# Kernel optimization log

Measured on AMD Instinct MI355X. Metric: run time of the kernel, lower is better.

The kernel has to match this reference:

```python
import jax, jax.numpy as jnp
import numpy as np

PH, PW = 7, 7      # pool_shape
SCALE = 1.0        # spatial_scale of PrRoIPool2D


def _tent_int(t):
    """Antiderivative of the bilinear tent kernel max(0, 1-|t|), clipped.
    Integral of tent from -inf to t."""
    t = jnp.clip(t, -1.0, 1.0)
    return jnp.where(t < 0.0, 0.5 * (t + 1.0) ** 2, 1.0 - 0.5 * (1.0 - t) ** 2)


def _axis_weights(lo, hi, n_bins, size):
    """Exact per-pixel integration weights along one axis.
    lo, hi: [R] roi edges. Returns (w [R, n_bins, size], bin_size [R]).
    w[r,k,i] = integral over bin k of tent(x - i) dx, so that
    sum_i F[i] * w[r,k,i] is the exact integral of the linearly
    interpolated signal F over bin k (Precise RoI Pooling)."""
    binsz = (hi - lo) / n_bins                       # [R]
    k = jnp.arange(n_bins, dtype=lo.dtype)
    a = lo[:, None] + k[None, :] * binsz[:, None]    # [R, n_bins] bin starts
    b = a + binsz[:, None]                           # bin ends
    i = jnp.arange(size, dtype=lo.dtype)             # pixel coordinates
    w = _tent_int(b[:, :, None] - i[None, None, :]) - _tent_int(a[:, :, None] - i[None, None, :])
    return w, binsz


def setup_inputs() -> dict:
    key = jax.random.key(0)
    k1, k2, k3, k4, k5 = jax.random.split(key, 5)
    B, C, H, W = 8, 64, 64, 64
    N = 512  # rois per leading dim; total R = N * B = 4096
    feature = jax.random.normal(k1, (B, C, H, W), dtype=jnp.float32)
    bidx = jax.random.randint(k2, (N, B, 1, 1), 0, B).astype(jnp.float32)
    x1 = jax.random.uniform(k3, (N, B, 1, 1), minval=0.0, maxval=W - 12.0)
    y1 = jax.random.uniform(k4, (N, B, 1, 1), minval=0.0, maxval=H - 12.0)
    wh = jax.random.uniform(k5, (N, B, 1, 1, 2), minval=4.0, maxval=12.0)
    x2 = x1 + wh[..., 0]
    y2 = y1 + wh[..., 1]
    rois = jnp.stack([bidx, x1, y1, x2, y2], axis=-1)  # [N, B, 1, 1, 5]
    return {"feature": feature, "rois": rois}


def reference(feature, rois):
    B, C, H, W = feature.shape
    # rois.permute([1,0,2,3,4]).reshape(-1, 5)
    r = jnp.transpose(rois, (1, 0, 2, 3, 4)).reshape(-1, 5)  # [R, 5]
    bidx = r[:, 0].astype(jnp.int32)
    x1 = r[:, 1] * SCALE
    y1 = r[:, 2] * SCALE
    x2 = r[:, 3] * SCALE
    y2 = r[:, 4] * SCALE

    wx, bw = _axis_weights(x1, x2, PW, W)  # [R, PW, W], [R]
    wy, bh = _axis_weights(y1, y2, PH, H)  # [R, PH, H], [R]

    # Route each ROI to its feature-batch entry without materializing
    # a [R, C, H, W] gather: fold the batch one-hot into the y-weights.
    onehot = (bidx[:, None] == jnp.arange(B)[None, :]).astype(feature.dtype)  # [R, B]
    wy_b = wy[:, :, None, :] * onehot[:, None, :, None]                      # [R, PH, B, H]

    tmp = jnp.einsum('rubi,bcij->rucj', wy_b, feature)  # [R, PH, C, W]
    integ = jnp.einsum('rucj,rvj->rcuv', tmp, wx)       # [R, C, PH, PW]

    area = jnp.maximum(bw * bh, 0.0)[:, None, None, None]
    bins = jnp.where(area > 0, integ / jnp.maximum(area, 1e-12), 0.0)

    # AvgPool2d(pool_shape) over the full (PH, PW) grid -> [R, C, 1, 1]
    out = jnp.mean(bins, axis=(2, 3), keepdims=True)
    return out
```

## Files before the change

kernel.cpp:

```cpp
#include <hip/hip_runtime.h>

constexpr int B = 8, C = 64, H = 64, W = 64;
constexpr int N = 512;
constexpr int R = N * B;
constexpr int HW = H * W;

__device__ __forceinline__ float tent_int(float t) {
    t = fminf(1.0f, fmaxf(-1.0f, t));
    float u = t + 1.0f;
    float v = 1.0f - t;
    return (t < 0.0f) ? 0.5f * u * u : 1.0f - 0.5f * v * v;
}

__device__ __forceinline__ float bf_lo(unsigned int u) {
    union { unsigned int i; float f; } c; c.i = u << 16; return c.f;
}
__device__ __forceinline__ float bf_hi(unsigned int u) {
    union { unsigned int i; float f; } c; c.i = u & 0xFFFF0000u; return c.f;
}
__device__ __forceinline__ unsigned short f2bf(float x) {
    union { float f; unsigned int i; } c; c.f = x;
    unsigned int r = c.i + 0x7FFFu + ((c.i >> 16) & 1u);
    return (unsigned short)(r >> 16);
}

__global__ __launch_bounds__(256) void transpose_kernel(
    const float* __restrict__ in,
    unsigned short* __restrict__ out)
{
    __shared__ float tile[64][65];
    const int b  = blockIdx.x >> 6;
    const int tp = (blockIdx.x & 63) * 64;
    const int t  = threadIdx.x;
    const int tq = t >> 6;
    const int tl = t & 63;

    const float* src = in + (size_t)b * C * HW;
    #pragma unroll
    for (int s = 0; s < 16; ++s) {
        int c = s * 4 + tq;
        tile[c][tl] = src[(size_t)c * HW + tp + tl];
    }
    __syncthreads();
    unsigned short* dst = out + ((size_t)b * HW + tp) * C;
    #pragma unroll
    for (int s = 0; s < 16; ++s) {
        int p = s * 4 + tq;
        dst[(size_t)p * C + tl] = f2bf(tile[tl][p]);
    }
}

__global__ __launch_bounds__(64) void prroi_main(
    const unsigned short* __restrict__ ft,
    const float* __restrict__ rois,
    float* __restrict__ out)
{
    const int r    = blockIdx.x;
    const int lane = threadIdx.x & 63;
    const int pg   = lane >> 3;
    const int cg   = lane & 7;

    const int bo = r >> 9;
    const int n  = r & 511;
    const float* rp = rois + ((size_t)n * B + bo) * 5;

    const int   b  = (int)rp[0];
    const float x1 = rp[1], y1 = rp[2], x2 = rp[3], y2 = rp[4];

    const int i_lo = max(0, (int)ceilf(y1 - 1.0f));
    const int i_hi = min(H - 1, (int)floorf(y2 + 1.0f));
    const int j_lo = max(0, (int)ceilf(x1 - 1.0f));
    const int j_hi = min(W - 1, (int)floorf(x2 + 1.0f));
    const int ny = i_hi - i_lo + 1;
    const int nx = j_hi - j_lo + 1;
    const int nk = (nx + 7) >> 3;

    float wx[2];
    int   coff[2];
    #pragma unroll
    for (int k = 0; k < 2; ++k) {
        const int  jj    = k * 8 + pg;
        const int  j     = j_lo + jj;
        const bool valid = (jj < nx);
        const float jf   = (float)j;
        wx[k]   = valid ? (tent_int(x2 - jf) - tent_int(x1 - jf)) : 0.0f;
        coff[k] = min(j, W - 1) * C + cg * 8;
    }

    float acc[8] = {0.f, 0.f, 0.f, 0.f, 0.f, 0.f, 0.f, 0.f};
    const unsigned short* fb = ft + ((size_t)b * HW + (size_t)i_lo * W) * C;
    for (int ii = 0; ii < ny; ++ii) {
        const float fi = (float)(i_lo + ii);
        const float wy = tent_int(y2 - fi) - tent_int(y1 - fi);
        const unsigned short* rowp = fb + (size_t)ii * (W * C);
        #pragma unroll 2
        for (int k = 0; k < nk; ++k) {
            const uint4 u = *reinterpret_cast<const uint4*>(rowp + coff[k]);
            const float w = wy * wx[k];
            acc[0] = fmaf(w, bf_lo(u.x), acc[0]);
            acc[1] = fmaf(w, bf_hi(u.x), acc[1]);
            acc[2] = fmaf(w, bf_lo(u.y), acc[2]);
            acc[3] = fmaf(w, bf_hi(u.y), acc[3]);
            acc[4] = fmaf(w, bf_lo(u.z), acc[4]);
            acc[5] = fmaf(w, bf_hi(u.z), acc[5]);
            acc[6] = fmaf(w, bf_lo(u.w), acc[6]);
            acc[7] = fmaf(w, bf_hi(u.w), acc[7]);
        }
    }

    #pragma unroll
    for (int e = 0; e < 8; ++e) {
        acc[e] += __shfl_xor(acc[e], 8);
        acc[e] += __shfl_xor(acc[e], 16);
        acc[e] += __shfl_xor(acc[e], 32);
    }

    const float prod  = (x2 - x1) * (y2 - y1);
    const float scale = (prod > 0.0f) ? (1.0f / fmaxf(prod, 49e-12f)) : 0.0f;

    if (lane < 8) {
        float* op = out + (size_t)r * C + lane * 8;
        float4 lo = make_float4(acc[0] * scale, acc[1] * scale,
                                acc[2] * scale, acc[3] * scale);
        float4 hi = make_float4(acc[4] * scale, acc[5] * scale,
                                acc[6] * scale, acc[7] * scale);
        *reinterpret_cast<float4*>(op)     = lo;
        *reinterpret_cast<float4*>(op + 4) = hi;
    }
}

__global__ __launch_bounds__(64) void prroi_fallback(
    const float* __restrict__ feature, const float* __restrict__ rois,
    float* __restrict__ out)
{
    const int r  = blockIdx.x;
    const int bo = r / N;
    const int n  = r - bo * N;
    const float* rp = rois + ((size_t)n * B + bo) * 5;
    const float x1 = rp[1], y1 = rp[2], x2 = rp[3], y2 = rp[4];
    const int b = (int)rp[0];
    int i_lo = max(0, (int)ceilf(y1 - 1.0f));
    int i_hi = min(H - 1, (int)floorf(y2 + 1.0f));
    int j_lo = max(0, (int)ceilf(x1 - 1.0f));
    int j_hi = min(W - 1, (int)floorf(x2 + 1.0f));
    const int ny = i_hi - i_lo + 1;
    const int nx = j_hi - j_lo + 1;
    __shared__ float sWy[16], sWx[16];
    const int t = threadIdx.x;
    if (t < 16) {
        int i = i_lo + t;
        sWy[t] = (t < ny) ? (tent_int(y2 - (float)i) - tent_int(y1 - (float)i)) : 0.0f;
    } else if (t < 32) {
        int tt = t - 16, j = j_lo + tt;
        sWx[tt] = (tt < nx) ? (tent_int(x2 - (float)j) - tent_int(x1 - (float)j)) : 0.0f;
    }
    __syncthreads();
    const float* fb = feature + ((size_t)b * C + t) * HW;
    float acc = 0.0f;
    for (int ii = 0; ii < ny; ++ii) {
        const float* row = fb + (size_t)(i_lo + ii) * W + j_lo;
        float rowsum = 0.0f;
        for (int jj = 0; jj < nx; ++jj) rowsum = fmaf(sWx[jj], row[jj], rowsum);
        acc = fmaf(sWy[ii], rowsum, acc);
    }
    const float bw = (x2 - x1) * (1.0f / 7.0f), bh = (y2 - y1) * (1.0f / 7.0f);
    const float area = fmaxf(bw * bh, 0.0f);
    out[(size_t)r * C + t] = (area > 0.0f) ? (acc / (49.0f * fmaxf(area, 1e-12f))) : 0.0f;
}

extern "C" void kernel_launch(void* const* d_in, const int* in_sizes, int n_in,
                              void* d_out, int out_size, void* d_ws, size_t ws_size,
                              hipStream_t stream) {
    const float* feature = (const float*)d_in[0];
    const float* rois    = (const float*)d_in[1];
    float* out           = (float*)d_out;

    const size_t need = (size_t)B * HW * C * sizeof(unsigned short);
    if (ws_size >= need) {
        unsigned short* ft = (unsigned short*)d_ws;
        transpose_kernel<<<B * (HW / 64), 256, 0, stream>>>(feature, ft);
        prroi_main<<<R, 64, 0, stream>>>(ft, rois, out);
    } else {
        prroi_fallback<<<R, 64, 0, stream>>>(feature, rois, out);
    }
}
```

Baseline: 71.35 us.

## Fuse transpose and pooling into one cooperative kernel with grid sync

Merges the bf16 channel-last transpose and the PrRoI pooling into a single cooperative kernel of 1024 blocks of 256 threads. Each block transposes a 32-pixel tile, then does a grid-wide sync before each of its four wavefronts pools one ROI. This removes a second kernel launch and the gap between the two kernels. In exchange it adds a grid barrier and a threadfence, needs every block to be resident at once, and falls back to the two-kernel path if the cooperative launch fails.

```diff
diff --git a/kernel.cpp b/kernel.cpp
--- a/kernel.cpp
+++ b/kernel.cpp
@@ -1,4 +1,7 @@
 #include <hip/hip_runtime.h>
+#include <hip/hip_cooperative_groups.h>
+
+namespace cg = cooperative_groups;
 
 constexpr int B = 8, C = 64, H = 64, W = 64;
 constexpr int N = 512;
@@ -22,6 +25,112 @@
     union { float f; unsigned int i; } c; c.f = x;
     unsigned int r = c.i + 0x7FFFu + ((c.i >> 16) & 1u);
     return (unsigned short)(r >> 16);
+}
+
+__global__ __launch_bounds__(256, 4) void prroi_fused(
+    const float* __restrict__ feature,
+    const float* __restrict__ rois,
+    unsigned short* __restrict__ ft,
+    float* __restrict__ out)
+{
+    __shared__ float tile[64][33];
+    {
+        const int b  = blockIdx.x >> 7;
+        const int tp = (blockIdx.x & 127) * 32;
+        const int t  = threadIdx.x;
+        const int tq8  = t >> 5;
+        const int tl32 = t & 31;
+        const float* src = feature + (size_t)b * C * HW;
+        #pragma unroll
+        for (int s = 0; s < 8; ++s) {
+            int c = s * 8 + tq8;
+            tile[c][tl32] = src[(size_t)c * HW + tp + tl32];
+        }
+        __syncthreads();
+        unsigned short* dst = ft + ((size_t)b * HW + tp) * C;
+        const int tq4  = t >> 6;
+        const int tl64 = t & 63;
+        #pragma unroll
+        for (int s = 0; s < 8; ++s) {
+            int p = s * 4 + tq4;
+            dst[(size_t)p * C + tl64] = f2bf(tile[tl64][p]);
+        }
+    }
+    __threadfence();
+    cg::this_grid().sync();
+
+    const int r    = blockIdx.x * 4 + (threadIdx.x >> 6);
+    const int lane = threadIdx.x & 63;
+    const int pg   = lane >> 3;
+    const int cg_  = lane & 7;
+
+    const int bo = r >> 9;
+    const int n  = r & 511;
+    const float* rp = rois + ((size_t)n * B + bo) * 5;
+
+    const int   b  = (int)rp[0];
+    const float x1 = rp[1], y1 = rp[2], x2 = rp[3], y2 = rp[4];
+
+    const int i_lo = max(0, (int)ceilf(y1 - 1.0f));
+    const int i_hi = min(H - 1, (int)floorf(y2 + 1.0f));
+    const int j_lo = max(0, (int)ceilf(x1 - 1.0f));
+    const int j_hi = min(W - 1, (int)floorf(x2 + 1.0f));
+    const int ny = i_hi - i_lo + 1;
+    const int nx = j_hi - j_lo + 1;
+    const int nk = (nx + 7) >> 3;
+
+    float wx[2];
+    int   coff[2];
+    #pragma unroll
+    for (int k = 0; k < 2; ++k) {
+        const int  jj    = k * 8 + pg;
+        const int  j     = j_lo + jj;
+        const bool valid = (jj < nx);
+        const float jf   = (float)j;
+        wx[k]   = valid ? (tent_int(x2 - jf) - tent_int(x1 - jf)) : 0.0f;
+        coff[k] = min(j, W - 1) * C + cg_ * 8;
+    }
+
+    float acc[8] = {0.f, 0.f, 0.f, 0.f, 0.f, 0.f, 0.f, 0.f};
+    const unsigned short* fb = ft + ((size_t)b * HW + (size_t)i_lo * W) * C;
+    for (int ii = 0; ii < ny; ++ii) {
+        const float fi = (float)(i_lo + ii);
+        const float wy = tent_int(y2 - fi) - tent_int(y1 - fi);
+        const unsigned short* rowp = fb + (size_t)ii * (W * C);
+        #pragma unroll 2
+        for (int k = 0; k < nk; ++k) {
+            const uint4 u = *reinterpret_cast<const uint4*>(rowp + coff[k]);
+            const float w = wy * wx[k];
+            acc[0] = fmaf(w, bf_lo(u.x), acc[0]);
+            acc[1] = fmaf(w, bf_hi(u.x), acc[1]);
+            acc[2] = fmaf(w, bf_lo(u.y), acc[2]);
+            acc[3] = fmaf(w, bf_hi(u.y), acc[3]);
+            acc[4] = fmaf(w, bf_lo(u.z), acc[4]);
+            acc[5] = fmaf(w, bf_hi(u.z), acc[5]);
+            acc[6] = fmaf(w, bf_lo(u.w), acc[6]);
+            acc[7] = fmaf(w, bf_hi(u.w), acc[7]);
+        }
+    }
+
+    #pragma unroll
+    for (int e = 0; e < 8; ++e) {
+        acc[e] += __shfl_xor(acc[e], 8);
+        acc[e] += __shfl_xor(acc[e], 16);
+        acc[e] += __shfl_xor(acc[e], 32);
+    }
+
+    const float prod  = (x2 - x1) * (y2 - y1);
+    const float scale = (prod > 0.0f) ? (1.0f / fmaxf(prod, 49e-12f)) : 0.0f;
+
+    if (lane < 8) {
+        float* op = out + (size_t)r * C + lane * 8;
+        float4 lo = make_float4(acc[0] * scale, acc[1] * scale,
+                                acc[2] * scale, acc[3] * scale);
+        float4 hi = make_float4(acc[4] * scale, acc[5] * scale,
+                                acc[6] * scale, acc[7] * scale);
+        *reinterpret_cast<float4*>(op)     = lo;
+        *reinterpret_cast<float4*>(op + 4) = hi;
+    }
 }
 
 __global__ __launch_bounds__(256) void transpose_kernel(
@@ -58,7 +167,7 @@
     const int r    = blockIdx.x;
     const int lane = threadIdx.x & 63;
     const int pg   = lane >> 3;
-    const int cg   = lane & 7;
+    const int cg_  = lane & 7;
 
     const int bo = r >> 9;
     const int n  = r & 511;
@@ -84,7 +193,7 @@
         const bool valid = (jj < nx);
         const float jf   = (float)j;
         wx[k]   = valid ? (tent_int(x2 - jf) - tent_int(x1 - jf)) : 0.0f;
-        coff[k] = min(j, W - 1) * C + cg * 8;
+        coff[k] = min(j, W - 1) * C + cg_ * 8;
     }
 
     float acc[8] = {0.f, 0.f, 0.f, 0.f, 0.f, 0.f, 0.f, 0.f};
@@ -178,8 +287,14 @@
     const size_t need = (size_t)B * HW * C * sizeof(unsigned short);
     if (ws_size >= need) {
         unsigned short* ft = (unsigned short*)d_ws;
-        transpose_kernel<<<B * (HW / 64), 256, 0, stream>>>(feature, ft);
-        prroi_main<<<R, 64, 0, stream>>>(ft, rois, out);
+        void* args[4] = { (void*)&feature, (void*)&rois, (void*)&ft, (void*)&out };
+        hipError_t e = hipLaunchCooperativeKernel(
+            (const void*)prroi_fused, dim3(1024), dim3(256), args, 0, stream);
+        if (e != hipSuccess) {
+            (void)hipGetLastError();
+            transpose_kernel<<<B * (HW / 64), 256, 0, stream>>>(feature, ft);
+            prroi_main<<<R, 64, 0, stream>>>(ft, rois, out);
+        }
     } else {
         prroi_fallback<<<R, 64, 0, stream>>>(feature, rois, out);
     }
```

New measurement: 206.2 us. +189.0%, slower.

## Split ROI rows across two waves with register prefetch of next row

Applied to the files above, without the earlier changes.

The per-ROI block grows from one wave to two. Each wave handles alternate feature rows and prefetches the next row's two column loads into registers before doing the FMAs, so memory latency overlaps with compute. The inner column loop is fully unrolled to always process two 8-column groups, and the partial sums of the two waves are combined through shared memory behind a barrier. This adds more waves and loads of invalid columns whose weight is zero, plus a synchronisation step, in exchange for more memory-level parallelism.

```diff
diff --git a/kernel.cpp b/kernel.cpp
--- a/kernel.cpp
+++ b/kernel.cpp
@@ -50,15 +50,17 @@
     }
 }
 
-__global__ __launch_bounds__(64) void prroi_main(
+__global__ __launch_bounds__(128) void prroi_main2(
     const unsigned short* __restrict__ ft,
     const float* __restrict__ rois,
     float* __restrict__ out)
 {
     const int r    = blockIdx.x;
-    const int lane = threadIdx.x & 63;
+    const int t    = threadIdx.x;
+    const int wid  = t >> 6;
+    const int lane = t & 63;
     const int pg   = lane >> 3;
-    const int cg   = lane & 7;
+    const int cg_  = lane & 7;
 
     const int bo = r >> 9;
     const int n  = r & 511;
@@ -73,7 +75,6 @@
     const int j_hi = min(W - 1, (int)floorf(x2 + 1.0f));
     const int ny = i_hi - i_lo + 1;
     const int nx = j_hi - j_lo + 1;
-    const int nk = (nx + 7) >> 3;
 
     float wx[2];
     int   coff[2];
@@ -84,28 +85,44 @@
         const bool valid = (jj < nx);
         const float jf   = (float)j;
         wx[k]   = valid ? (tent_int(x2 - jf) - tent_int(x1 - jf)) : 0.0f;
-        coff[k] = min(j, W - 1) * C + cg * 8;
+        coff[k] = min(j, W - 1) * C + cg_ * 8;
     }
 
     float acc[8] = {0.f, 0.f, 0.f, 0.f, 0.f, 0.f, 0.f, 0.f};
     const unsigned short* fb = ft + ((size_t)b * HW + (size_t)i_lo * W) * C;
-    for (int ii = 0; ii < ny; ++ii) {
+
+    uint4 c0, c1;
+    {
+        const unsigned short* rowp = fb + (size_t)min(wid, ny - 1) * (W * C);
+        c0 = *reinterpret_cast<const uint4*>(rowp + coff[0]);
+        c1 = *reinterpret_cast<const uint4*>(rowp + coff[1]);
+    }
+    for (int ii = wid; ii < ny; ii += 2) {
+        const unsigned short* rown = fb + (size_t)min(ii + 2, ny - 1) * (W * C);
+        const uint4 n0 = *reinterpret_cast<const uint4*>(rown + coff[0]);
+        const uint4 n1 = *reinterpret_cast<const uint4*>(rown + coff[1]);
+
         const float fi = (float)(i_lo + ii);
         const float wy = tent_int(y2 - fi) - tent_int(y1 - fi);
-        const unsigned short* rowp = fb + (size_t)ii * (W * C);
-        #pragma unroll 2
-        for (int k = 0; k < nk; ++k) {
-            const uint4 u = *reinterpret_cast<const uint4*>(rowp + coff[k]);
-            const float w = wy * wx[k];
-            acc[0] = fmaf(w, bf_lo(u.x), acc[0]);
-            acc[1] = fmaf(w, bf_hi(u.x), acc[1]);
-            acc[2] = fmaf(w, bf_lo(u.y), acc[2]);
-            acc[3] = fmaf(w, bf_hi(u.y), acc[3]);
-            acc[4] = fmaf(w, bf_lo(u.z), acc[4]);
-            acc[5] = fmaf(w, bf_hi(u.z), acc[5]);
-            acc[6] = fmaf(w, bf_lo(u.w), acc[6]);
-            acc[7] = fmaf(w, bf_hi(u.w), acc[7]);
-        }
+        const float w0 = wy * wx[0];
+        const float w1 = wy * wx[1];
+        acc[0] = fmaf(w0, bf_lo(c0.x), acc[0]);
+        acc[1] = fmaf(w0, bf_hi(c0.x), acc[1]);
+        acc[2] = fmaf(w0, bf_lo(c0.y), acc[2]);
+        acc[3] = fmaf(w0, bf_hi(c0.y), acc[3]);
+        acc[4] = fmaf(w0, bf_lo(c0.z), acc[4]);
+        acc[5] = fmaf(w0, bf_hi(c0.z), acc[5]);
+        acc[6] = fmaf(w0, bf_lo(c0.w), acc[6]);
+        acc[7] = fmaf(w0, bf_hi(c0.w), acc[7]);
+        acc[0] = fmaf(w1, bf_lo(c1.x), acc[0]);
+        acc[1] = fmaf(w1, bf_hi(c1.x), acc[1]);
+        acc[2] = fmaf(w1, bf_lo(c1.y), acc[2]);
+        acc[3] = fmaf(w1, bf_hi(c1.y), acc[3]);
+        acc[4] = fmaf(w1, bf_lo(c1.z), acc[4]);
+        acc[5] = fmaf(w1, bf_hi(c1.z), acc[5]);
+        acc[6] = fmaf(w1, bf_lo(c1.w), acc[6]);
+        acc[7] = fmaf(w1, bf_hi(c1.w), acc[7]);
+        c0 = n0; c1 = n1;
     }
 
     #pragma unroll
@@ -115,15 +132,21 @@
         acc[e] += __shfl_xor(acc[e], 32);
     }
 
-    const float prod  = (x2 - x1) * (y2 - y1);
-    const float scale = (prod > 0.0f) ? (1.0f / fmaxf(prod, 49e-12f)) : 0.0f;
-
-    if (lane < 8) {
+    __shared__ float part[64];
+    if (wid == 1 && lane < 8) {
+        #pragma unroll
+        for (int e = 0; e < 8; ++e) part[lane * 8 + e] = acc[e];
+    }
+    __syncthreads();
+    if (wid == 0 && lane < 8) {
+        const float prod  = (x2 - x1) * (y2 - y1);
+        const float scale = (prod > 0.0f) ? (1.0f / fmaxf(prod, 49e-12f)) : 0.0f;
+        const float* pp = part + lane * 8;
         float* op = out + (size_t)r * C + lane * 8;
-        float4 lo = make_float4(acc[0] * scale, acc[1] * scale,
-                                acc[2] * scale, acc[3] * scale);
-        float4 hi = make_float4(acc[4] * scale, acc[5] * scale,
-                                acc[6] * scale, acc[7] * scale);
+        float4 lo = make_float4((acc[0] + pp[0]) * scale, (acc[1] + pp[1]) * scale,
+                                (acc[2] + pp[2]) * scale, (acc[3] + pp[3]) * scale);
+        float4 hi = make_float4((acc[4] + pp[4]) * scale, (acc[5] + pp[5]) * scale,
+                                (acc[6] + pp[6]) * scale, (acc[7] + pp[7]) * scale);
         *reinterpret_cast<float4*>(op)     = lo;
         *reinterpret_cast<float4*>(op + 4) = hi;
     }
@@ -179,7 +202,7 @@
     if (ws_size >= need) {
         unsigned short* ft = (unsigned short*)d_ws;
         transpose_kernel<<<B * (HW / 64), 256, 0, stream>>>(feature, ft);
-        prroi_main<<<R, 64, 0, stream>>>(ft, rois, out);
+        prroi_main2<<<R, 128, 0, stream>>>(ft, rois, out);
     } else {
         prroi_fallback<<<R, 64, 0, stream>>>(feature, rois, out);
     }
```

After: 69.90 us. 1.02x faster.

## Drop bf16 transpose pass and read NCHW fp32 feature directly per ROI

Applied to the files above, without the earlier changes.

Removes the separate transpose-to-channels-last bf16 kernel and its workspace round trip. A single kernel now has 128 threads per ROI: 16 lanes cover x columns and 8 channel groups each handle 8 strided channels, reading fp32 NCHW rows directly. Partial sums are reduced with shuffles and gathered through shared memory for the store. This saves a launch and a full feature rewrite, but each load is a scattered 4-byte access spread over channel planes rather than a 16-byte vector. It also goes back to full fp32 precision.

```diff
diff --git a/kernel.cpp b/kernel.cpp
--- a/kernel.cpp
+++ b/kernel.cpp
@@ -12,53 +12,15 @@
     return (t < 0.0f) ? 0.5f * u * u : 1.0f - 0.5f * v * v;
 }
 
-__device__ __forceinline__ float bf_lo(unsigned int u) {
-    union { unsigned int i; float f; } c; c.i = u << 16; return c.f;
-}
-__device__ __forceinline__ float bf_hi(unsigned int u) {
-    union { unsigned int i; float f; } c; c.i = u & 0xFFFF0000u; return c.f;
-}
-__device__ __forceinline__ unsigned short f2bf(float x) {
-    union { float f; unsigned int i; } c; c.f = x;
-    unsigned int r = c.i + 0x7FFFu + ((c.i >> 16) & 1u);
-    return (unsigned short)(r >> 16);
-}
-
-__global__ __launch_bounds__(256) void transpose_kernel(
-    const float* __restrict__ in,
-    unsigned short* __restrict__ out)
-{
-    __shared__ float tile[64][65];
-    const int b  = blockIdx.x >> 6;
-    const int tp = (blockIdx.x & 63) * 64;
-    const int t  = threadIdx.x;
-    const int tq = t >> 6;
-    const int tl = t & 63;
-
-    const float* src = in + (size_t)b * C * HW;
-    #pragma unroll
-    for (int s = 0; s < 16; ++s) {
-        int c = s * 4 + tq;
-        tile[c][tl] = src[(size_t)c * HW + tp + tl];
-    }
-    __syncthreads();
-    unsigned short* dst = out + ((size_t)b * HW + tp) * C;
-    #pragma unroll
-    for (int s = 0; s < 16; ++s) {
-        int p = s * 4 + tq;
-        dst[(size_t)p * C + tl] = f2bf(tile[tl][p]);
-    }
-}
-
-__global__ __launch_bounds__(64) void prroi_main(
-    const unsigned short* __restrict__ ft,
+__global__ __launch_bounds__(128) void prroi_direct(
+    const float* __restrict__ feature,
     const float* __restrict__ rois,
     float* __restrict__ out)
 {
     const int r    = blockIdx.x;
-    const int lane = threadIdx.x & 63;
-    const int pg   = lane >> 3;
-    const int cg   = lane & 7;
+    const int t    = threadIdx.x;
+    const int cgrp = t >> 4;
+    const int j16  = t & 15;
 
     const int bo = r >> 9;
     const int n  = r & 511;
@@ -73,99 +35,49 @@
     const int j_hi = min(W - 1, (int)floorf(x2 + 1.0f));
     const int ny = i_hi - i_lo + 1;
     const int nx = j_hi - j_lo + 1;
-    const int nk = (nx + 7) >> 3;
 
-    float wx[2];
-    int   coff[2];
-    #pragma unroll
-    for (int k = 0; k < 2; ++k) {
-        const int  jj    = k * 8 + pg;
-        const int  j     = j_lo + jj;
-        const bool valid = (jj < nx);
-        const float jf   = (float)j;
-        wx[k]   = valid ? (tent_int(x2 - jf) - tent_int(x1 - jf)) : 0.0f;
-        coff[k] = min(j, W - 1) * C + cg * 8;
-    }
+    const int   j   = j_lo + j16;
+    const float jf  = (float)j;
+    const float wxl = (j16 < nx) ? (tent_int(x2 - jf) - tent_int(x1 - jf)) : 0.0f;
+    const int   jcl = min(j, W - 1);
+
+    const float* p0 = feature + ((size_t)b * C + cgrp) * HW
+                              + (size_t)i_lo * W + jcl;
 
     float acc[8] = {0.f, 0.f, 0.f, 0.f, 0.f, 0.f, 0.f, 0.f};
-    const unsigned short* fb = ft + ((size_t)b * HW + (size_t)i_lo * W) * C;
     for (int ii = 0; ii < ny; ++ii) {
         const float fi = (float)(i_lo + ii);
         const float wy = tent_int(y2 - fi) - tent_int(y1 - fi);
-        const unsigned short* rowp = fb + (size_t)ii * (W * C);
-        #pragma unroll 2
-        for (int k = 0; k < nk; ++k) {
-            const uint4 u = *reinterpret_cast<const uint4*>(rowp + coff[k]);
-            const float w = wy * wx[k];
-            acc[0] = fmaf(w, bf_lo(u.x), acc[0]);
-            acc[1] = fmaf(w, bf_hi(u.x), acc[1]);
-            acc[2] = fmaf(w, bf_lo(u.y), acc[2]);
-            acc[3] = fmaf(w, bf_hi(u.y), acc[3]);
-            acc[4] = fmaf(w, bf_lo(u.z), acc[4]);
-            acc[5] = fmaf(w, bf_hi(u.z), acc[5]);
-            acc[6] = fmaf(w, bf_lo(u.w), acc[6]);
-            acc[7] = fmaf(w, bf_hi(u.w), acc[7]);
-        }
+        const float w  = wy * wxl;
+        const float* prow = p0 + (size_t)ii * W;
+        float v[8];
+        #pragma unroll
+        for (int co = 0; co < 8; ++co)
+            v[co] = prow[(size_t)co * 8 * HW];
+        #pragma unroll
+        for (int co = 0; co < 8; ++co)
+            acc[co] = fmaf(w, v[co], acc[co]);
     }
 
     #pragma unroll
-    for (int e = 0; e < 8; ++e) {
-        acc[e] += __shfl_xor(acc[e], 8);
-        acc[e] += __shfl_xor(acc[e], 16);
-        acc[e] += __shfl_xor(acc[e], 32);
+    for (int co = 0; co < 8; ++co) {
+        acc[co] += __shfl_xor(acc[co], 1);
+        acc[co] += __shfl_xor(acc[co], 2);
+        acc[co] += __shfl_xor(acc[co], 4);
+        acc[co] += __shfl_xor(acc[co], 8);
     }
 
     const float prod  = (x2 - x1) * (y2 - y1);
     const float scale = (prod > 0.0f) ? (1.0f / fmaxf(prod, 49e-12f)) : 0.0f;
 
-    if (lane < 8) {
-        float* op = out + (size_t)r * C + lane * 8;
-        float4 lo = make_float4(acc[0] * scale, acc[1] * scale,
-                                acc[2] * scale, acc[3] * scale);
-        float4 hi = make_float4(acc[4] * scale, acc[5] * scale,
-                                acc[6] * scale, acc[7] * scale);
-        *reinterpret_cast<float4*>(op)     = lo;
-        *reinterpret_cast<float4*>(op + 4) = hi;
-    }
-}
-
-__global__ __launch_bounds__(64) void prroi_fallback(
-    const float* __restrict__ feature, const float* __restrict__ rois,
-    float* __restrict__ out)
-{
-    const int r  = blockIdx.x;
-    const int bo = r / N;
-    const int n  = r - bo * N;
-    const float* rp = rois + ((size_t)n * B + bo) * 5;
-    const float x1 = rp[1], y1 = rp[2], x2 = rp[3], y2 = rp[4];
-    const int b = (int)rp[0];
-    int i_lo = max(0, (int)ceilf(y1 - 1.0f));
-    int i_hi = min(H - 1, (int)floorf(y2 + 1.0f));
-    int j_lo = max(0, (int)ceilf(x1 - 1.0f));
-    int j_hi = min(W - 1, (int)floorf(x2 + 1.0f));
-    const int ny = i_hi - i_lo + 1;
-    const int nx = j_hi - j_lo + 1;
-    __shared__ float sWy[16], sWx[16];
-    const int t = threadIdx.x;
-    if (t < 16) {
-        int i = i_lo + t;
-        sWy[t] = (t < ny) ? (tent_int(y2 - (float)i) - tent_int(y1 - (float)i)) : 0.0f;
-    } else if (t < 32) {
-        int tt = t - 16, j = j_lo + tt;
-        sWx[tt] = (tt < nx) ? (tent_int(x2 - (float)j) - tent_int(x1 - (float)j)) : 0.0f;
+    __shared__ float obuf[64];
+    if (j16 == 0) {
+        #pragma unroll
+        for (int co = 0; co < 8; ++co)
+            obuf[co * 8 + cgrp] = acc[co] * scale;
     }
     __syncthreads();
-    const float* fb = feature + ((size_t)b * C + t) * HW;
-    float acc = 0.0f;
-    for (int ii = 0; ii < ny; ++ii) {
-        const float* row = fb + (size_t)(i_lo + ii) * W + j_lo;
-        float rowsum = 0.0f;
-        for (int jj = 0; jj < nx; ++jj) rowsum = fmaf(sWx[jj], row[jj], rowsum);
-        acc = fmaf(sWy[ii], rowsum, acc);
-    }
-    const float bw = (x2 - x1) * (1.0f / 7.0f), bh = (y2 - y1) * (1.0f / 7.0f);
-    const float area = fmaxf(bw * bh, 0.0f);
-    out[(size_t)r * C + t] = (area > 0.0f) ? (acc / (49.0f * fmaxf(area, 1e-12f))) : 0.0f;
+    if (t < 64) out[(size_t)r * C + t] = obuf[t];
 }
 
 extern "C" void kernel_launch(void* const* d_in, const int* in_sizes, int n_in,
@@ -174,13 +86,7 @@
     const float* feature = (const float*)d_in[0];
     const float* rois    = (const float*)d_in[1];
     float* out           = (float*)d_out;
+    (void)d_ws; (void)ws_size;
 
-    const size_t need = (size_t)B * HW * C * sizeof(unsigned short);
-    if (ws_size >= need) {
-        unsigned short* ft = (unsigned short*)d_ws;
-        transpose_kernel<<<B * (HW / 64), 256, 0, stream>>>(feature, ft);
-        prroi_main<<<R, 64, 0, stream>>>(ft, rois, out);
-    } else {
-        prroi_fallback<<<R, 64, 0, stream>>>(feature, rois, out);
-    }
+    prroi_direct<<<R, 128, 0, stream>>>(feature, rois, out);
 }
```

New measurement: 89.46 us. 1.25x slower.
